# Kernel optimization log

Hardware: AMD Instinct MI355X
Metric: run time of the kernel (lower is better)

Reference implementation:

```python
import jax, jax.numpy as jnp
import numpy as np

N, E, D, O = 50000, 800000, 128, 128
BN_EPS = 1e-5

def setup_inputs() -> dict:
    key = jax.random.key(0)
    ks = jax.random.split(key, 12)
    s1 = 1.0 / np.sqrt(D)
    s2 = 1.0 / np.sqrt(O)
    return {
        "x": jax.random.normal(ks[0], (N, D), dtype=jnp.float32),
        "edge_index": jax.random.randint(ks[1], (2, E), 0, N, dtype=jnp.int64),
        "batch": jnp.zeros((N,), dtype=jnp.int64),
        "eps": jnp.float32(0.0),  # GINConv train_eps parameter, init 0
        "W1": jax.random.uniform(ks[2], (O, D), jnp.float32, -s1, s1),
        "b1": jax.random.uniform(ks[3], (O,), jnp.float32, -s1, s1),
        "gamma1": jnp.ones((O,), jnp.float32),
        "beta1": jnp.zeros((O,), jnp.float32),
        "W2": jax.random.uniform(ks[4], (O, O), jnp.float32, -s2, s2),
        "b2": jax.random.uniform(ks[5], (O,), jnp.float32, -s2, s2),
        "gamma2": jnp.ones((O,), jnp.float32),
        "beta2": jnp.zeros((O,), jnp.float32),
    }

def _bn(h, gamma, beta):
    # BatchNorm1d training mode: biased variance over nodes
    m = jnp.mean(h, axis=0)
    v = jnp.var(h, axis=0)
    return (h - m) * jax.lax.rsqrt(v + BN_EPS) * gamma + beta

def reference(x, edge_index, batch, eps, W1, b1, gamma1, beta1, W2, b2, gamma2, beta2):
    src, dst = edge_index[0], edge_index[1]
    # sum_{j in N(i)} x_j  (scatter-add over edges)
    agg = jax.ops.segment_sum(x[src], dst, num_segments=N)
    h = (1.0 + eps) * x + agg
    h = jax.nn.relu(_bn(h @ W1.T + b1, gamma1, beta1))
    h = jax.nn.relu(_bn(h @ W2.T + b2, gamma2, beta2))
    return h
```

## Files before the change

kernel.cpp:

```cpp
#include <hip/hip_runtime.h>
#include <hip/hip_bf16.h>

typedef __hip_bfloat16 bf16;
typedef unsigned short u16;
typedef unsigned int u32;
typedef __attribute__((ext_vector_type(8))) short short8;
typedef __attribute__((ext_vector_type(4))) float floatx4;

#define N_NODES 50000
#define N_EDGES 800000
#define DIM 128
#define NB2 1563
#define NB2A 1792
#define CAP2 768
#define T_EDGES 4096
#define WROW 136
#define WIMG (128 * WROW)

__device__ __forceinline__ u16 f2bfbits(float f) {
    bf16 h = __float2bfloat16(f);
    return *(u16*)&h;
}
__device__ __forceinline__ unsigned pack2(float a, float b) {
    return (unsigned)f2bfbits(a) | ((unsigned)f2bfbits(b) << 16);
}
__device__ __forceinline__ float lo2f(u32 u) { u32 v = u << 16; return __builtin_bit_cast(float, v); }
__device__ __forceinline__ float hi2f(u32 u) { u32 v = u & 0xFFFF0000u; return __builtin_bit_cast(float, v); }
__device__ __forceinline__ float b162f(u16 u) { u32 v = (u32)u << 16; return __builtin_bit_cast(float, v); }

__global__ void prep_kernel(const float* __restrict__ x, u32* __restrict__ xb,
                            const int* __restrict__ ei, int* __restrict__ flags,
                            int* __restrict__ gcur, float* __restrict__ stats,
                            const float* __restrict__ W1, const float* __restrict__ W2,
                            u16* __restrict__ w1i, u16* __restrict__ w2i) {
    int t = threadIdx.x;
    int bid = blockIdx.x;
    if (bid >= 3125) {
        const float* W = (bid == 3125) ? W1 : W2;
        u16* wi = (bid == 3125) ? w1i : w2i;
        #pragma unroll 4
        for (int j = 0; j < 68; j++) {
            int q = j * 256 + t;
            int r = q / WROW, c = q - r * WROW;
            wi[q] = (c < 128) ? f2bfbits(W[r * 128 + c]) : (u16)0;
        }
        return;
    }
    if (bid == 0) {
        __shared__ int sdet;
        #pragma unroll
        for (int j = 0; j < 7; j++) {
            int i = j * 256 + t;
            if (i < NB2) gcur[i * 16] = 0;
        }
        #pragma unroll
        for (int j = 0; j < 16; j++) stats[j * 256 + t] = 0.f;
        if (t == 0) sdet = 0;
        __syncthreads();
        if (t < 64) { if (ei[2 * t + 1] != 0) atomicOr(&sdet, 1); }
        __syncthreads();
        if (t == 0) flags[1] = (sdet == 0) ? 1 : 0;
    }
    int i = (bid * 256 + t) * 8;
    floatx4 v0 = *(const floatx4*)&x[i];
    floatx4 v1 = *(const floatx4*)&x[i + 4];
    uint4 r;
    r.x = pack2(v0[0], v0[1]); r.y = pack2(v0[2], v0[3]);
    r.z = pack2(v1[0], v1[1]); r.w = pack2(v1[2], v1[3]);
    *(uint4*)&xb[i / 2] = r;
}

__launch_bounds__(256)
__global__ void sort1_kernel(const int* __restrict__ ei, const int* __restrict__ flags,
                             u32* __restrict__ gbuck, int* __restrict__ gcur) {
    __shared__ int hist[NB2A];
    __shared__ int cur[NB2A];
    __shared__ int gbase[NB2A];
    int t = threadIdx.x;
    int is64 = flags[1];
    int e0 = blockIdx.x * T_EDGES;
    int n = N_EDGES - e0; if (n > T_EDGES) n = T_EDGES;

    for (int i = t; i < NB2A; i += 256) { hist[i] = 0; cur[i] = 0; }
    __syncthreads();

    u32 ed[T_EDGES / 256];
    #pragma unroll
    for (int j = 0; j < T_EDGES / 256; j++) {
        int idx = j * 256 + t;
        if (idx < n) {
            int e = e0 + idx;
            int js = e, jd = N_EDGES + e;
            if (is64) { js = 2 * e; jd = 2 * (N_EDGES + e); }
            u32 p = (u32)ei[js] | ((u32)ei[jd] << 16);
            ed[j] = p;
            atomicAdd(&hist[p >> 21], 1);
        }
    }
    __syncthreads();

    for (int i = t; i < NB2; i += 256) {
        int c = hist[i];
        gbase[i] = c ? atomicAdd(&gcur[i * 16], c) : 0;
    }
    __syncthreads();

    #pragma unroll
    for (int j = 0; j < T_EDGES / 256; j++) {
        int idx = j * 256 + t;
        if (idx < n) {
            u32 p = ed[j];
            int b = p >> 21;
            int pos = gbase[b] + atomicAdd(&cur[b], 1);
            gbuck[(long)b * CAP2 + pos] = p;
        }
    }
}

__launch_bounds__(256)
__global__ void sortagg_kernel(const u32* __restrict__ xb, const u32* __restrict__ gbuck,
                               const int* __restrict__ gcur, const float* __restrict__ epsp,
                               u32* __restrict__ hw) {
    __shared__ u32 sbuf[CAP2];
    __shared__ u16 slist[CAP2];
    __shared__ int cnt[32], offs[32], cur[32];
    int t = threadIdx.x, lane = t & 63, wv = t >> 6;
    int b = blockIdx.x;
    int n = gcur[b * 16]; if (n > CAP2) n = CAP2;
    long base = (long)b * CAP2;

    if (t < 32) { cnt[t] = 0; cur[t] = 0; }
    __syncthreads();
    for (int i = t; i < n; i += 256) {
        u32 p = gbuck[base + i];
        sbuf[i] = p;
        atomicAdd(&cnt[(p >> 16) & 31], 1);
    }
    __syncthreads();
    if (t < 32) {
        int v = cnt[t];
        int pv = v;
        #pragma unroll
        for (int d = 1; d < 32; d <<= 1) {
            int up = __shfl_up(pv, d);
            if (t >= d) pv += up;
        }
        offs[t] = pv - v;
    }
    __syncthreads();
    for (int i = t; i < n; i += 256) {
        u32 p = sbuf[i];
        int d = (p >> 16) & 31;
        int pos = offs[d] + atomicAdd(&cur[d], 1);
        slist[pos] = (u16)(p & 0xFFFF);
    }
    __syncthreads();

    float ep1 = 1.0f + epsp[0];
    for (int nn = wv; nn < 32; nn += 4) {
        int node = b * 32 + nn;
        if (node >= N_NODES) break;
        u32 self = xb[node * 64 + lane];
        float ax = ep1 * lo2f(self), ay = ep1 * hi2f(self);
        int s = offs[nn], e = s + cnt[nn];
        int i = s;
        for (; i + 8 <= e; i += 8) {
            int m[8];
            u32 u[8];
            #pragma unroll
            for (int j = 0; j < 8; j++) m[j] = slist[i + j];
            #pragma unroll
            for (int j = 0; j < 8; j++) u[j] = xb[m[j] * 64 + lane];
            #pragma unroll
            for (int j = 0; j < 8; j++) { ax += lo2f(u[j]); ay += hi2f(u[j]); }
        }
        for (; i + 2 <= e; i += 2) {
            u32 u0 = xb[(int)slist[i] * 64 + lane], u1 = xb[(int)slist[i + 1] * 64 + lane];
            ax += lo2f(u0) + lo2f(u1); ay += hi2f(u0) + hi2f(u1);
        }
        if (i < e) {
            u32 u = xb[(int)slist[i] * 64 + lane];
            ax += lo2f(u); ay += hi2f(u);
        }
        hw[node * 64 + lane] = pack2(ax, ay);
    }
}

template<int TRANSFORM>
__launch_bounds__(256)
__global__ void gemm_mfma(const u16* __restrict__ Ap, const u16* __restrict__ wimg,
                          const float* __restrict__ bias,
                          const float* __restrict__ gamma, const float* __restrict__ beta,
                          const float* __restrict__ gstat,
                          u16* __restrict__ Yp, float* __restrict__ ostat) {
    __shared__ u16 sW[WIMG];
    __shared__ float sScale[128], sShift[128], sBias[128], sSum[128], sSq[128];
    int t = threadIdx.x, lane = t & 63, wv = t >> 6;

    #pragma unroll
    for (int it = 0; it < 9; it++) {
        int q = it * 256 + t;
        if (q < WIMG / 8) {
            uint4 v = ((const uint4*)wimg)[q];
            *(uint4*)&sW[q * 8] = v;
        }
    }
    if (t < 128) {
        sSum[t] = 0.f; sSq[t] = 0.f; sBias[t] = bias[t];
        if (TRANSFORM) {
            float m = gstat[t * 16] * (1.0f / N_NODES);
            float v = fmaxf(gstat[t * 16 + 8] * (1.0f / N_NODES) - m * m, 0.0f);
            float rs = rsqrtf(v + 1e-5f);
            float sc = gamma[t] * rs;
            sScale[t] = sc;
            sShift[t] = beta[t] - m * sc;
        }
    }
    __syncthreads();

    int col0 = lane & 15, quad = lane >> 4;
    int row0 = blockIdx.x * 128 + wv * 32;

    short8 afr[2][4];
    #pragma unroll
    for (int tt = 0; tt < 2; tt++) {
        int mrow = row0 + tt * 16 + col0;
        #pragma unroll
        for (int ks = 0; ks < 4; ks++)
            afr[tt][ks] = *(const short8*)&Ap[mrow * DIM + ks * 32 + quad * 8];
    }
    if (TRANSFORM) {
        #pragma unroll
        for (int tt = 0; tt < 2; tt++) {
            #pragma unroll
            for (int ks = 0; ks < 4; ks++) {
                int kb = ks * 32 + quad * 8;
                short8 a = afr[tt][ks], r;
                #pragma unroll
                for (int j = 0; j < 8; j++) {
                    float f = b162f((u16)a[j]);
                    r[j] = (short)f2bfbits(fmaxf(fmaf(f, sScale[kb + j], sShift[kb + j]), 0.f));
                }
                afr[tt][ks] = r;
            }
        }
    }

    floatx4 acc[2][8];
    #pragma unroll
    for (int tt = 0; tt < 2; tt++)
        #pragma unroll
        for (int nt = 0; nt < 8; nt++) acc[tt][nt] = (floatx4){0.f, 0.f, 0.f, 0.f};

    #pragma unroll
    for (int ks = 0; ks < 4; ks++) {
        #pragma unroll
        for (int nt = 0; nt < 8; nt++) {
            short8 bfr = *(const short8*)&sW[(nt * 16 + col0) * WROW + ks * 32 + quad * 8];
            acc[0][nt] = __builtin_amdgcn_mfma_f32_16x16x32_bf16(afr[0][ks], bfr, acc[0][nt], 0, 0, 0);
            acc[1][nt] = __builtin_amdgcn_mfma_f32_16x16x32_bf16(afr[1][ks], bfr, acc[1][nt], 0, 0, 0);
        }
    }

    #pragma unroll
    for (int tt = 0; tt < 2; tt++) {
        int rtile = row0 + tt * 16;
        if (rtile >= N_NODES) break;
        #pragma unroll
        for (int nt = 0; nt < 8; nt++) {
            int col = nt * 16 + col0;
            float bb = sBias[col];
            float o0 = acc[tt][nt][0] + bb, o1 = acc[tt][nt][1] + bb;
            float o2 = acc[tt][nt][2] + bb, o3 = acc[tt][nt][3] + bb;
            int rbase = rtile + quad * 4;
            Yp[(rbase + 0) * DIM + col] = f2bfbits(o0);
            Yp[(rbase + 1) * DIM + col] = f2bfbits(o1);
            Yp[(rbase + 2) * DIM + col] = f2bfbits(o2);
            Yp[(rbase + 3) * DIM + col] = f2bfbits(o3);
            float s = o0 + o1 + o2 + o3;
            float q = o0 * o0 + o1 * o1 + o2 * o2 + o3 * o3;
            s += __shfl_xor(s, 16); s += __shfl_xor(s, 32);
            q += __shfl_xor(q, 16); q += __shfl_xor(q, 32);
            if (quad == 0) { atomicAdd(&sSum[col], s); atomicAdd(&sSq[col], q); }
        }
    }
    __syncthreads();
    if (t < 128) {
        atomicAdd(&ostat[t * 16], sSum[t]);
        atomicAdd(&ostat[t * 16 + 8], sSq[t]);
    }
}

__global__ void output_kernel(const u32* __restrict__ Y,
                              const float* __restrict__ gstat,
                              const float* __restrict__ gamma, const float* __restrict__ beta,
                              float* __restrict__ out) {
    __shared__ float sScale[128], sShift[128];
    int t = threadIdx.x;
    if (t < 128) {
        float m = gstat[t * 16] * (1.0f / N_NODES);
        float v = fmaxf(gstat[t * 16 + 8] * (1.0f / N_NODES) - m * m, 0.0f);
        float rs = rsqrtf(v + 1e-5f);
        float sc = gamma[t] * rs;
        sScale[t] = sc;
        sShift[t] = beta[t] - m * sc;
    }
    __syncthreads();
    int i = (blockIdx.x * 256 + t) * 8;
    int c = i & 127;
    uint4 v = *(const uint4*)&Y[i / 2];
    u32 w[4] = {v.x, v.y, v.z, v.w};
    floatx4 o0, o1;
    #pragma unroll
    for (int j = 0; j < 4; j++) {
        float lo = lo2f(w[j]), hi = hi2f(w[j]);
        float r0 = fmaxf(fmaf(lo, sScale[c + 2 * j],     sShift[c + 2 * j]),     0.f);
        float r1 = fmaxf(fmaf(hi, sScale[c + 2 * j + 1], sShift[c + 2 * j + 1]), 0.f);
        if (j < 2) { o0[2 * j] = r0; o0[2 * j + 1] = r1; }
        else       { o1[2 * (j - 2)] = r0; o1[2 * (j - 2) + 1] = r1; }
    }
    *(floatx4*)&out[i] = o0;
    *(floatx4*)&out[i + 4] = o1;
}

extern "C" void kernel_launch(void* const* d_in, const int* in_sizes, int n_in,
                              void* d_out, int out_size, void* d_ws, size_t ws_size,
                              hipStream_t stream) {
    const float* x   = (const float*)d_in[0];
    const int* eraw  = (const int*)d_in[1];
    const float* eps = (const float*)d_in[3];
    const float* W1  = (const float*)d_in[4];
    const float* b1  = (const float*)d_in[5];
    const float* g1  = (const float*)d_in[6];
    const float* be1 = (const float*)d_in[7];
    const float* W2  = (const float*)d_in[8];
    const float* b2  = (const float*)d_in[9];
    const float* g2  = (const float*)d_in[10];
    const float* be2 = (const float*)d_in[11];

    char* ws = (char*)d_ws;
    size_t off = 0;
    u32* xb = (u32*)(ws + off);          off += (size_t)N_NODES * DIM * 2;
    u32* h1 = (u32*)(ws + off);          off += (size_t)N_NODES * DIM * 2;
    u16* y1 = (u16*)(ws + off);          off += (size_t)N_NODES * DIM * 2;
    u16* y2 = (u16*)(ws + off);          off += (size_t)N_NODES * DIM * 2;
    float* stats = (float*)(ws + off);   off += 4096 * 4;
    float* st1 = stats;
    float* st2 = stats + 2048;
    u16* w1i = (u16*)(ws + off);         off += (size_t)WIMG * 2;
    u16* w2i = (u16*)(ws + off);         off += (size_t)WIMG * 2;
    u32* gbuck = (u32*)(ws + off);       off += (size_t)NB2 * CAP2 * 4;
    int* gcur = (int*)(ws + off);        off += (size_t)((NB2 * 16 + 255) & ~255) * 4;
    int* flags = (int*)(ws + off);       off += 16 * 4;

    prep_kernel<<<3127, 256, 0, stream>>>(x, xb, eraw, flags, gcur, stats, W1, W2, w1i, w2i);
    sort1_kernel<<<(N_EDGES + T_EDGES - 1) / T_EDGES, 256, 0, stream>>>(eraw, flags, gbuck, gcur);
    sortagg_kernel<<<NB2, 256, 0, stream>>>(xb, gbuck, gcur, eps, h1);

    const int gemmGrid = (N_NODES + 127) / 128;
    gemm_mfma<0><<<gemmGrid, 256, 0, stream>>>((const u16*)h1, w1i, b1,
                                               nullptr, nullptr, nullptr, y1, st1);
    gemm_mfma<1><<<gemmGrid, 256, 0, stream>>>(y1, w2i, b2,
                                               g1, be1, st1, y2, st2);
    output_kernel<<<N_NODES * DIM / (8 * 256), 256, 0, stream>>>((const u32*)y2, st2,
                                                                 g2, be2, (float*)d_out);
}
```

Baseline: 240.4 us.

## Fuse aggregation with first GEMM and merge prep with edge bucketing

Merges the prep and sort1 kernels into one launch, where each edge-sorting block detects the index width itself instead of reading a flag. The zeroing of counters and stats moves to hipMemsetAsync. The aggregation kernel now writes each 32-node tile to shared memory and runs the first MFMA GEMM with BN stats in place, which removes the h1 round-trip through global memory and one launch. In exchange, the W1 fragments are read from global/L2 per block instead of staged in LDS, the GEMM tile is small (32 rows), and the memsets add two stream operations.

```diff
diff --git a/kernel.cpp b/kernel.cpp
--- a/kernel.cpp
+++ b/kernel.cpp
@@ -14,6 +14,8 @@
 #define NB2A 1792
 #define CAP2 768
 #define T_EDGES 4096
+#define NT1 196
+#define XCHUNKS 3125
 #define WROW 136
 #define WIMG (128 * WROW)
 
@@ -28,101 +30,87 @@
 __device__ __forceinline__ float hi2f(u32 u) { u32 v = u & 0xFFFF0000u; return __builtin_bit_cast(float, v); }
 __device__ __forceinline__ float b162f(u16 u) { u32 v = (u32)u << 16; return __builtin_bit_cast(float, v); }
 
-__global__ void prep_kernel(const float* __restrict__ x, u32* __restrict__ xb,
-                            const int* __restrict__ ei, int* __restrict__ flags,
-                            int* __restrict__ gcur, float* __restrict__ stats,
-                            const float* __restrict__ W1, const float* __restrict__ W2,
-                            u16* __restrict__ w1i, u16* __restrict__ w2i) {
-    int t = threadIdx.x;
-    int bid = blockIdx.x;
-    if (bid >= 3125) {
-        const float* W = (bid == 3125) ? W1 : W2;
-        u16* wi = (bid == 3125) ? w1i : w2i;
+__launch_bounds__(256)
+__global__ void k1_kernel(const float* __restrict__ x, const int* __restrict__ ei,
+                          u32* __restrict__ xb,
+                          const float* __restrict__ W1, const float* __restrict__ W2,
+                          u16* __restrict__ w1i, u16* __restrict__ w2i,
+                          u32* __restrict__ gbuck, int* __restrict__ gcur) {
+    __shared__ int hist[NB2A];
+    __shared__ int cur[NB2A];
+    __shared__ int gbase[NB2A];
+    __shared__ int sdet;
+    int t = threadIdx.x, bid = blockIdx.x;
+
+    if (bid < NT1) {
+        if (t == 0) sdet = 0;
+        for (int i = t; i < NB2A; i += 256) { hist[i] = 0; cur[i] = 0; }
+        __syncthreads();
+        if (t < 64) { if (ei[2 * t + 1] != 0) atomicOr(&sdet, 1); }
+        __syncthreads();
+        int is64 = (sdet == 0);
+        int e0 = bid * T_EDGES;
+        int n = N_EDGES - e0; if (n > T_EDGES) n = T_EDGES;
+        u32 ed[T_EDGES / 256];
+        #pragma unroll
+        for (int j = 0; j < T_EDGES / 256; j++) {
+            int idx = j * 256 + t;
+            if (idx < n) {
+                int e = e0 + idx;
+                int js = e, jd = N_EDGES + e;
+                if (is64) { js = 2 * e; jd = 2 * (N_EDGES + e); }
+                u32 p = (u32)ei[js] | ((u32)ei[jd] << 16);
+                ed[j] = p;
+                atomicAdd(&hist[p >> 21], 1);
+            }
+        }
+        __syncthreads();
+        for (int i = t; i < NB2; i += 256) {
+            int c = hist[i];
+            gbase[i] = c ? atomicAdd(&gcur[i * 16], c) : 0;
+        }
+        __syncthreads();
+        #pragma unroll
+        for (int j = 0; j < T_EDGES / 256; j++) {
+            int idx = j * 256 + t;
+            if (idx < n) {
+                u32 p = ed[j];
+                int b = p >> 21;
+                int pos = gbase[b] + atomicAdd(&cur[b], 1);
+                gbuck[(long)b * CAP2 + pos] = p;
+            }
+        }
+    } else if (bid < NT1 + XCHUNKS) {
+        int uu = bid - NT1;
+        int i = (uu * 256 + t) * 8;
+        floatx4 v0 = *(const floatx4*)&x[i];
+        floatx4 v1 = *(const floatx4*)&x[i + 4];
+        uint4 r;
+        r.x = pack2(v0[0], v0[1]); r.y = pack2(v0[2], v0[3]);
+        r.z = pack2(v1[0], v1[1]); r.w = pack2(v1[2], v1[3]);
+        *(uint4*)&xb[i / 2] = r;
+    } else {
+        int which = bid - NT1 - XCHUNKS;
+        const float* W = which ? W2 : W1;
+        u16* wi = which ? w2i : w1i;
         #pragma unroll 4
         for (int j = 0; j < 68; j++) {
             int q = j * 256 + t;
             int r = q / WROW, c = q - r * WROW;
             wi[q] = (c < 128) ? f2bfbits(W[r * 128 + c]) : (u16)0;
         }
-        return;
-    }
-    if (bid == 0) {
-        __shared__ int sdet;
-        #pragma unroll
-        for (int j = 0; j < 7; j++) {
-            int i = j * 256 + t;
-            if (i < NB2) gcur[i * 16] = 0;
-        }
-        #pragma unroll
-        for (int j = 0; j < 16; j++) stats[j * 256 + t] = 0.f;
-        if (t == 0) sdet = 0;
-        __syncthreads();
-        if (t < 64) { if (ei[2 * t + 1] != 0) atomicOr(&sdet, 1); }
-        __syncthreads();
-        if (t == 0) flags[1] = (sdet == 0) ? 1 : 0;
-    }
-    int i = (bid * 256 + t) * 8;
-    floatx4 v0 = *(const floatx4*)&x[i];
-    floatx4 v1 = *(const floatx4*)&x[i + 4];
-    uint4 r;
-    r.x = pack2(v0[0], v0[1]); r.y = pack2(v0[2], v0[3]);
-    r.z = pack2(v1[0], v1[1]); r.w = pack2(v1[2], v1[3]);
-    *(uint4*)&xb[i / 2] = r;
+    }
 }
 
 __launch_bounds__(256)
-__global__ void sort1_kernel(const int* __restrict__ ei, const int* __restrict__ flags,
-                             u32* __restrict__ gbuck, int* __restrict__ gcur) {
-    __shared__ int hist[NB2A];
-    __shared__ int cur[NB2A];
-    __shared__ int gbase[NB2A];
-    int t = threadIdx.x;
-    int is64 = flags[1];
-    int e0 = blockIdx.x * T_EDGES;
-    int n = N_EDGES - e0; if (n > T_EDGES) n = T_EDGES;
-
-    for (int i = t; i < NB2A; i += 256) { hist[i] = 0; cur[i] = 0; }
-    __syncthreads();
-
-    u32 ed[T_EDGES / 256];
-    #pragma unroll
-    for (int j = 0; j < T_EDGES / 256; j++) {
-        int idx = j * 256 + t;
-        if (idx < n) {
-            int e = e0 + idx;
-            int js = e, jd = N_EDGES + e;
-            if (is64) { js = 2 * e; jd = 2 * (N_EDGES + e); }
-            u32 p = (u32)ei[js] | ((u32)ei[jd] << 16);
-            ed[j] = p;
-            atomicAdd(&hist[p >> 21], 1);
-        }
-    }
-    __syncthreads();
-
-    for (int i = t; i < NB2; i += 256) {
-        int c = hist[i];
-        gbase[i] = c ? atomicAdd(&gcur[i * 16], c) : 0;
-    }
-    __syncthreads();
-
-    #pragma unroll
-    for (int j = 0; j < T_EDGES / 256; j++) {
-        int idx = j * 256 + t;
-        if (idx < n) {
-            u32 p = ed[j];
-            int b = p >> 21;
-            int pos = gbase[b] + atomicAdd(&cur[b], 1);
-            gbuck[(long)b * CAP2 + pos] = p;
-        }
-    }
-}
-
-__launch_bounds__(256)
-__global__ void sortagg_kernel(const u32* __restrict__ xb, const u32* __restrict__ gbuck,
-                               const int* __restrict__ gcur, const float* __restrict__ epsp,
-                               u32* __restrict__ hw) {
+__global__ void aggGemm1_kernel(const u32* __restrict__ xb, const u32* __restrict__ gbuck,
+                                const int* __restrict__ gcur, const float* __restrict__ epsp,
+                                const u16* __restrict__ w1i, const float* __restrict__ bias,
+                                u16* __restrict__ y1, float* __restrict__ ostat) {
     __shared__ u32 sbuf[CAP2];
     __shared__ u16 slist[CAP2];
+    __shared__ u16 h1t[32 * WROW];
+    __shared__ float sSum[128], sSq[128];
     __shared__ int cnt[32], offs[32], cur[32];
     int t = threadIdx.x, lane = t & 63, wv = t >> 6;
     int b = blockIdx.x;
@@ -130,6 +118,10 @@
     long base = (long)b * CAP2;
 
     if (t < 32) { cnt[t] = 0; cur[t] = 0; }
+    if (t < 128) { sSum[t] = 0.f; sSq[t] = 0.f; }
+    if (b == NB2 - 1) {
+        for (int i = t; i < 16 * WROW / 2; i += 256) ((u32*)h1t)[16 * WROW / 2 + i] = 0;
+    }
     __syncthreads();
     for (int i = t; i < n; i += 256) {
         u32 p = gbuck[base + i];
@@ -138,13 +130,9 @@
     }
     __syncthreads();
     if (t < 32) {
-        int v = cnt[t];
-        int pv = v;
-        #pragma unroll
-        for (int d = 1; d < 32; d <<= 1) {
-            int up = __shfl_up(pv, d);
-            if (t >= d) pv += up;
-        }
+        int v = cnt[t], pv = v;
+        #pragma unroll
+        for (int d = 1; d < 32; d <<= 1) { int up = __shfl_up(pv, d); if (t >= d) pv += up; }
         offs[t] = pv - v;
     }
     __syncthreads();
@@ -165,34 +153,77 @@
         int s = offs[nn], e = s + cnt[nn];
         int i = s;
         for (; i + 8 <= e; i += 8) {
-            int m[8];
-            u32 u[8];
+            int m[8]; u32 uv[8];
             #pragma unroll
             for (int j = 0; j < 8; j++) m[j] = slist[i + j];
             #pragma unroll
-            for (int j = 0; j < 8; j++) u[j] = xb[m[j] * 64 + lane];
+            for (int j = 0; j < 8; j++) uv[j] = xb[m[j] * 64 + lane];
             #pragma unroll
-            for (int j = 0; j < 8; j++) { ax += lo2f(u[j]); ay += hi2f(u[j]); }
+            for (int j = 0; j < 8; j++) { ax += lo2f(uv[j]); ay += hi2f(uv[j]); }
         }
         for (; i + 2 <= e; i += 2) {
             u32 u0 = xb[(int)slist[i] * 64 + lane], u1 = xb[(int)slist[i + 1] * 64 + lane];
             ax += lo2f(u0) + lo2f(u1); ay += hi2f(u0) + hi2f(u1);
         }
         if (i < e) {
-            u32 u = xb[(int)slist[i] * 64 + lane];
-            ax += lo2f(u); ay += hi2f(u);
-        }
-        hw[node * 64 + lane] = pack2(ax, ay);
-    }
-}
-
-template<int TRANSFORM>
+            u32 u0 = xb[(int)slist[i] * 64 + lane];
+            ax += lo2f(u0); ay += hi2f(u0);
+        }
+        *(u32*)&h1t[nn * WROW + 2 * lane] = pack2(ax, ay);
+    }
+    __syncthreads();
+
+    int col0 = lane & 15, quad = lane >> 4;
+    int rt = wv & 1, ng = wv >> 1;
+    short8 afr[4];
+    #pragma unroll
+    for (int ks = 0; ks < 4; ks++)
+        afr[ks] = *(const short8*)&h1t[(rt * 16 + col0) * WROW + ks * 32 + quad * 8];
+    floatx4 acc[4];
+    #pragma unroll
+    for (int j = 0; j < 4; j++) acc[j] = (floatx4){0.f, 0.f, 0.f, 0.f};
+    #pragma unroll
+    for (int ks = 0; ks < 4; ks++) {
+        #pragma unroll
+        for (int j = 0; j < 4; j++) {
+            int nt = ng * 4 + j;
+            short8 bfr = *(const short8*)&w1i[(nt * 16 + col0) * WROW + ks * 32 + quad * 8];
+            acc[j] = __builtin_amdgcn_mfma_f32_16x16x32_bf16(afr[ks], bfr, acc[j], 0, 0, 0);
+        }
+    }
+    int rtile = b * 32 + rt * 16;
+    if (rtile < N_NODES) {
+        #pragma unroll
+        for (int j = 0; j < 4; j++) {
+            int col = (ng * 4 + j) * 16 + col0;
+            float bb = bias[col];
+            float o0 = acc[j][0] + bb, o1 = acc[j][1] + bb;
+            float o2 = acc[j][2] + bb, o3 = acc[j][3] + bb;
+            int rbase = rtile + quad * 4;
+            y1[(rbase + 0) * DIM + col] = f2bfbits(o0);
+            y1[(rbase + 1) * DIM + col] = f2bfbits(o1);
+            y1[(rbase + 2) * DIM + col] = f2bfbits(o2);
+            y1[(rbase + 3) * DIM + col] = f2bfbits(o3);
+            float s = o0 + o1 + o2 + o3;
+            float q = o0 * o0 + o1 * o1 + o2 * o2 + o3 * o3;
+            s += __shfl_xor(s, 16); s += __shfl_xor(s, 32);
+            q += __shfl_xor(q, 16); q += __shfl_xor(q, 32);
+            if (quad == 0) { atomicAdd(&sSum[col], s); atomicAdd(&sSq[col], q); }
+        }
+    }
+    __syncthreads();
+    if (t < 128) {
+        atomicAdd(&ostat[t * 16], sSum[t]);
+        atomicAdd(&ostat[t * 16 + 8], sSq[t]);
+    }
+}
+
 __launch_bounds__(256)
-__global__ void gemm_mfma(const u16* __restrict__ Ap, const u16* __restrict__ wimg,
-                          const float* __restrict__ bias,
-                          const float* __restrict__ gamma, const float* __restrict__ beta,
-                          const float* __restrict__ gstat,
-                          u16* __restrict__ Yp, float* __restrict__ ostat) {
+__global__ void gemm2_kernel(const u16* __restrict__ Ap, const u16* __restrict__ wimg,
+                             const float* __restrict__ bias,
+                             const float* __restrict__ gamma, const float* __restrict__ beta,
+                             const float* __restrict__ gstat,
+                             u16* __restrict__ Yp, float* __restrict__ ostat) {
     __shared__ u16 sW[WIMG];
     __shared__ float sScale[128], sShift[128], sBias[128], sSum[128], sSq[128];
     int t = threadIdx.x, lane = t & 63, wv = t >> 6;
@@ -200,21 +231,16 @@
     #pragma unroll
     for (int it = 0; it < 9; it++) {
         int q = it * 256 + t;
-        if (q < WIMG / 8) {
-            uint4 v = ((const uint4*)wimg)[q];
-            *(uint4*)&sW[q * 8] = v;
-        }
+        if (q < WIMG / 8) *(uint4*)&sW[q * 8] = ((const uint4*)wimg)[q];
     }
     if (t < 128) {
         sSum[t] = 0.f; sSq[t] = 0.f; sBias[t] = bias[t];
-        if (TRANSFORM) {
-            float m = gstat[t * 16] * (1.0f / N_NODES);
-            float v = fmaxf(gstat[t * 16 + 8] * (1.0f / N_NODES) - m * m, 0.0f);
-            float rs = rsqrtf(v + 1e-5f);
-            float sc = gamma[t] * rs;
-            sScale[t] = sc;
-            sShift[t] = beta[t] - m * sc;
-        }
+        float m = gstat[t * 16] * (1.0f / N_NODES);
+        float v = fmaxf(gstat[t * 16 + 8] * (1.0f / N_NODES) - m * m, 0.0f);
+        float rs = rsqrtf(v + 1e-5f);
+        float sc = gamma[t] * rs;
+        sScale[t] = sc;
+        sShift[t] = beta[t] - m * sc;
     }
     __syncthreads();
 
@@ -225,42 +251,38 @@
     #pragma unroll
     for (int tt = 0; tt < 2; tt++) {
         int mrow = row0 + tt * 16 + col0;
+        if (mrow > N_NODES - 1) mrow = N_NODES - 1;
         #pragma unroll
         for (int ks = 0; ks < 4; ks++)
             afr[tt][ks] = *(const short8*)&Ap[mrow * DIM + ks * 32 + quad * 8];
     }
-    if (TRANSFORM) {
-        #pragma unroll
-        for (int tt = 0; tt < 2; tt++) {
+    #pragma unroll
+    for (int tt = 0; tt < 2; tt++)
+        #pragma unroll
+        for (int ks = 0; ks < 4; ks++) {
+            int kb = ks * 32 + quad * 8;
+            short8 a = afr[tt][ks], r;
             #pragma unroll
-            for (int ks = 0; ks < 4; ks++) {
-                int kb = ks * 32 + quad * 8;
-                short8 a = afr[tt][ks], r;
-                #pragma unroll
-                for (int j = 0; j < 8; j++) {
-                    float f = b162f((u16)a[j]);
-                    r[j] = (short)f2bfbits(fmaxf(fmaf(f, sScale[kb + j], sShift[kb + j]), 0.f));
-                }
-                afr[tt][ks] = r;
+            for (int j = 0; j < 8; j++) {
+                float f = b162f((u16)a[j]);
+                r[j] = (short)f2bfbits(fmaxf(fmaf(f, sScale[kb + j], sShift[kb + j]), 0.f));
             }
-        }
-    }
+            afr[tt][ks] = r;
+        }
 
     floatx4 acc[2][8];
     #pragma unroll
     for (int tt = 0; tt < 2; tt++)
         #pragma unroll
         for (int nt = 0; nt < 8; nt++) acc[tt][nt] = (floatx4){0.f, 0.f, 0.f, 0.f};
-
-    #pragma unroll
-    for (int ks = 0; ks < 4; ks++) {
+    #pragma unroll
+    for (int ks = 0; ks < 4; ks++)
         #pragma unroll
         for (int nt = 0; nt < 8; nt++) {
             short8 bfr = *(const short8*)&sW[(nt * 16 + col0) * WROW + ks * 32 + quad * 8];
             acc[0][nt] = __builtin_amdgcn_mfma_f32_16x16x32_bf16(afr[0][ks], bfr, acc[0][nt], 0, 0, 0);
             acc[1][nt] = __builtin_amdgcn_mfma_f32_16x16x32_bf16(afr[1][ks], bfr, acc[1][nt], 0, 0, 0);
         }
-    }
 
     #pragma unroll
     for (int tt = 0; tt < 2; tt++) {
@@ -341,7 +363,6 @@
     char* ws = (char*)d_ws;
     size_t off = 0;
     u32* xb = (u32*)(ws + off);          off += (size_t)N_NODES * DIM * 2;
-    u32* h1 = (u32*)(ws + off);          off += (size_t)N_NODES * DIM * 2;
     u16* y1 = (u16*)(ws + off);          off += (size_t)N_NODES * DIM * 2;
     u16* y2 = (u16*)(ws + off);          off += (size_t)N_NODES * DIM * 2;
     float* stats = (float*)(ws + off);   off += 4096 * 4;
@@ -351,17 +372,13 @@
     u16* w2i = (u16*)(ws + off);         off += (size_t)WIMG * 2;
     u32* gbuck = (u32*)(ws + off);       off += (size_t)NB2 * CAP2 * 4;
     int* gcur = (int*)(ws + off);        off += (size_t)((NB2 * 16 + 255) & ~255) * 4;
-    int* flags = (int*)(ws + off);       off += 16 * 4;
-
-    prep_kernel<<<3127, 256, 0, stream>>>(x, xb, eraw, flags, gcur, stats, W1, W2, w1i, w2i);
-    sort1_kernel<<<(N_EDGES + T_EDGES - 1) / T_EDGES, 256, 0, stream>>>(eraw, flags, gbuck, gcur);
-    sortagg_kernel<<<NB2, 256, 0, stream>>>(xb, gbuck, gcur, eps, h1);
-
-    const int gemmGrid = (N_NODES + 127) / 128;
-    gemm_mfma<0><<<gemmGrid, 256, 0, stream>>>((const u16*)h1, w1i, b1,
-                                               nullptr, nullptr, nullptr, y1, st1);
-    gemm_mfma<1><<<gemmGrid, 256, 0, stream>>>(y1, w2i, b2,
-                                               g1, be1, st1, y2, st2);
+
+    hipMemsetAsync(gcur, 0, (size_t)NB2 * 16 * 4, stream);
+    hipMemsetAsync(stats, 0, 4096 * 4, stream);
+
+    k1_kernel<<<NT1 + XCHUNKS + 2, 256, 0, stream>>>(x, eraw, xb, W1, W2, w1i, w2i, gbuck, gcur);
+    aggGemm1_kernel<<<NB2, 256, 0, stream>>>(xb, gbuck, gcur, eps, w1i, b1, y1, st1);
+    gemm2_kernel<<<(N_NODES + 127) / 128, 256, 0, stream>>>(y1, w2i, b2, g1, be1, st1, y2, st2);
     output_kernel<<<N_NODES * DIM / (8 * 256), 256, 0, stream>>>((const u32*)y2, st2,
                                                                  g2, be2, (float*)d_out);
 }
```

After: 272.9 us. 13.5% more time.
